# Kernel tuning notes

Measured on AMD Instinct MI355X. Metric: run time of the kernel, lower is better.

Reference implementation:

```python
import jax, jax.numpy as jnp
import numpy as np

B, L, H, N, A = 1024, 50, 256, 100000, 100

def setup_inputs() -> dict:
    key = jax.random.key(0)
    k1, k2, k3, k4, k5, k6 = jax.random.split(key, 6)
    stdv = 1.0 / np.sqrt(H)
    u = lambda k, shp: jax.random.uniform(k, shp, jnp.float32, -stdv, stdv)
    inputs = jax.random.randint(k1, (B, L), 0, N)
    masks = jnp.ones((B, L), jnp.float32)
    return {
        'inputs': inputs,
        'masks': masks,
        'emb': u(k2, (N, H)),
        'Qw': u(k3, (A, H)),
        'Kw': u(k4, (A, H)),
        'lin_w': u(k5, (H, 2 * H)),
        'lin_b': u(k6, (H,)),
    }

def reference(inputs, masks, emb, Qw, Kw, lin_w, lin_b):
    x = emb[inputs]                                   # [B,L,H]
    Q = jax.nn.sigmoid(jnp.einsum('blh,ah->bla', x, Qw))   # [B,L,A]
    K = jax.nn.sigmoid(jnp.einsum('blh,ah->bla', x, Kw))
    affinity = jnp.einsum('bla,bma->blm', Q, K) / jnp.sqrt(jnp.float32(A))  # [B,L,L]
    # remove diagonal (affinity - diag_embed(diagonal))
    eye = jnp.eye(L, dtype=affinity.dtype)
    masked_affinity = affinity * (1.0 - eye)
    col_masked = masked_affinity * masks[:, None, :]  # column mask
    item_score = jnp.sum(col_masked, axis=2) * masks  # [B,L]
    item_score = jax.nn.softmax(item_score, axis=1) * masks
    item_score = item_score / jnp.sum(item_score, axis=1, keepdims=True)
    att_final = jnp.sum(item_score[:, :, None] * x, axis=1)  # [B,H]
    # last valid item per session
    lengths = masks.sum(axis=1).astype(jnp.int32)
    last_id = jnp.take_along_axis(inputs, (lengths - 1)[:, None], axis=1)[:, 0]
    last_emb = emb[last_id]                           # [B,H]
    final_rep = jnp.concatenate([att_final, last_emb], axis=1) @ lin_w.T + lin_b  # [B,H]
    scores = final_rep @ emb[1:].T                    # [B,N-1]
    return scores, affinity
```

## Files before the change

### kernel.cpp

```cpp
#include <hip/hip_runtime.h>
#include <hip/hip_bf16.h>

#define BB 1024
#define LL 50
#define HH 256
#define AA 100
#define NN 100000
#define NM1 99999

typedef short short8 __attribute__((ext_vector_type(8)));
typedef float f32x4 __attribute__((ext_vector_type(4)));

__device__ __forceinline__ float wave_sum(float v) {
#pragma unroll
  for (int off = 32; off; off >>= 1) v += __shfl_xor(v, off, 64);
  return v;
}
__device__ __forceinline__ float wave_max(float v) {
#pragma unroll
  for (int off = 32; off; off >>= 1) v = fmaxf(v, __shfl_xor(v, off, 64));
  return v;
}
__device__ __forceinline__ short f2bf(float f) {
  union { __hip_bfloat16 h; short s; } u;
  u.h = __float2bfloat16(f);
  return u.s;
}
__device__ __forceinline__ float bf2f(short s) {
  union { short s; __hip_bfloat16 h; } u;
  u.s = s;
  return __bfloat162float(u.h);
}

__global__ __launch_bounds__(256) void session_kernel(
    const int* __restrict__ inputs, const float* __restrict__ masks,
    const float* __restrict__ emb, const float* __restrict__ Qw,
    const float* __restrict__ Kw, const float* __restrict__ lin_w,
    const float* __restrict__ lin_b, float* __restrict__ out_aff,
    short* __restrict__ frb) {
  __shared__ short s_xb[64 * 256];
  __shared__ short s_q[64 * 128];
  __shared__ short s_k[64 * 128];
  __shared__ float s_mask[64];
  __shared__ int s_idx[64];
  __shared__ float s_rowp[4][64];
  __shared__ float s_p[64];
  __shared__ float s_cat[2 * HH];
  __shared__ int s_last;

  const int b = blockIdx.x;
  const int tid = threadIdx.x;
  const int lane = tid & 63;
  const int wv = tid >> 6;
  const int l15 = lane & 15;
  const int lg = lane >> 4;

  if (tid < 64) s_mask[tid] = (tid < LL) ? masks[b * LL + tid] : 0.f;
  if (tid < LL) s_idx[tid] = inputs[b * LL + tid];
#pragma unroll
  for (int i = 0; i < 4; ++i) {
    short8 z = {};
    ((short8*)s_q)[tid + i * 256] = z;
    ((short8*)s_k)[tid + i * 256] = z;
  }
  __syncthreads();

  for (int u = tid; u < LL * 32; u += 256) {
    const int r = u >> 5, c = u & 31;
    const float* s = emb + (size_t)s_idx[r] * HH + c * 8;
    const float4 f0 = *(const float4*)s;
    const float4 f1 = *(const float4*)(s + 4);
    short8 v;
    v[0] = f2bf(f0.x); v[1] = f2bf(f0.y); v[2] = f2bf(f0.z); v[3] = f2bf(f0.w);
    v[4] = f2bf(f1.x); v[5] = f2bf(f1.y); v[6] = f2bf(f1.z); v[7] = f2bf(f1.w);
    const int byte = ((r << 9) | (c << 4)) ^ ((r & 7) << 4);
    *(short8*)((char*)s_xb + byte) = v;
  }
  __syncthreads();

  f32x4 acc[4][4];
#pragma unroll
  for (int i = 0; i < 4; ++i)
#pragma unroll
    for (int j = 0; j < 4; ++j) acc[i][j] = (f32x4)(0.f);

#pragma unroll
  for (int ks = 0; ks < 8; ++ks) {
    const int kb = (ks * 32 + lg * 8) * 2;
    short8 af[4];
#pragma unroll
    for (int mf = 0; mf < 4; ++mf) {
      const int r = mf * 16 + l15;
      af[mf] = *(const short8*)((const char*)s_xb +
                                (((r << 9) + kb) ^ ((r & 7) << 4)));
    }
#pragma unroll
    for (int nfi = 0; nfi < 4; ++nfi) {
      const int nf = wv + 4 * nfi;
      const float* Wp = (nf < 7) ? Qw : Kw;
      int arow = (nf < 7) ? nf * 16 + l15 : (nf - 7) * 16 + l15;
      if (nf >= 14) arow = 0;
      if (arow > AA - 1) arow = AA - 1;
      const float* s = Wp + (size_t)arow * HH + ks * 32 + lg * 8;
      const float4 w0 = *(const float4*)s;
      const float4 w1 = *(const float4*)(s + 4);
      short8 bf;
      bf[0] = f2bf(w0.x); bf[1] = f2bf(w0.y); bf[2] = f2bf(w0.z); bf[3] = f2bf(w0.w);
      bf[4] = f2bf(w1.x); bf[5] = f2bf(w1.y); bf[6] = f2bf(w1.z); bf[7] = f2bf(w1.w);
#pragma unroll
      for (int mf = 0; mf < 4; ++mf)
        acc[nfi][mf] =
            __builtin_amdgcn_mfma_f32_16x16x32_bf16(af[mf], bf, acc[nfi][mf], 0, 0, 0);
    }
  }
#pragma unroll
  for (int nfi = 0; nfi < 4; ++nfi) {
    const int nf = wv + 4 * nfi;
#pragma unroll
    for (int mf = 0; mf < 4; ++mf)
#pragma unroll
      for (int j = 0; j < 4; ++j) {
        const int row = mf * 16 + lg * 4 + j;
        const float sg = 1.f / (1.f + expf(-acc[nfi][mf][j]));
        if (row < LL && nf < 14) {
          if (nf < 7) {
            const int a = nf * 16 + l15;
            if (a < AA)
              *(short*)((char*)s_q + (((row << 8) + a * 2) ^ ((row & 7) << 4))) =
                  f2bf(sg);
          } else {
            const int a = (nf - 7) * 16 + l15;
            if (a < AA)
              *(short*)((char*)s_k + (((row << 8) + a * 2) ^ ((row & 7) << 4))) =
                  f2bf(sg);
          }
        }
      }
  }
  __syncthreads();

  f32x4 c4[4];
#pragma unroll
  for (int i = 0; i < 4; ++i) c4[i] = (f32x4)(0.f);
#pragma unroll
  for (int ks = 0; ks < 4; ++ks) {
    const int kb = (ks * 32 + lg * 8) * 2;
    const int mrow = wv * 16 + l15;
    const short8 kf = *(const short8*)((const char*)s_k +
                                       (((mrow << 8) + kb) ^ ((mrow & 7) << 4)));
#pragma unroll
    for (int mf = 0; mf < 4; ++mf) {
      const int r = mf * 16 + l15;
      const short8 qf = *(const short8*)((const char*)s_q +
                                         (((r << 8) + kb) ^ ((r & 7) << 4)));
      c4[mf] = __builtin_amdgcn_mfma_f32_16x16x32_bf16(qf, kf, c4[mf], 0, 0, 0);
    }
  }
  {
    const int col = wv * 16 + l15;
#pragma unroll
    for (int mf = 0; mf < 4; ++mf)
#pragma unroll
      for (int j = 0; j < 4; ++j) {
        const int row = mf * 16 + lg * 4 + j;
        const float val = c4[mf][j] * 0.1f;
        if (row < LL && col < LL)
          out_aff[(size_t)b * (LL * LL) + row * LL + col] = val;
        float am = (col < LL && col != row) ? val * s_mask[col] : 0.f;
        am += __shfl_xor(am, 1, 64);
        am += __shfl_xor(am, 2, 64);
        am += __shfl_xor(am, 4, 64);
        am += __shfl_xor(am, 8, 64);
        if (l15 == 0) s_rowp[wv][row] = am;
      }
  }
  __syncthreads();

  if (tid < 64) {
    const int l = tid;
    const float mk = s_mask[l];
    float v = -3.4e38f;
    if (l < LL)
      v = (s_rowp[0][l] + s_rowp[1][l] + s_rowp[2][l] + s_rowp[3][l]) * mk;
    const float mx = wave_max(v);
    const float e = (l < LL) ? expf(v - mx) : 0.f;
    const float s1 = wave_sum(e);
    float p = e / s1 * mk;
    const float s2 = wave_sum(p);
    p /= s2;
    if (l < LL) s_p[l] = p;
    const float cnt = wave_sum(mk);
    if (l == 0) s_last = s_idx[(int)(cnt + 0.5f) - 1];
  }
  __syncthreads();

  {
    const int h = tid;
    float a = 0.f;
#pragma unroll
    for (int l = 0; l < LL; ++l) {
      const short xv = *(const short*)((const char*)s_xb +
                                       ((((l << 9) + h * 2)) ^ ((l & 7) << 4)));
      a += s_p[l] * bf2f(xv);
    }
    s_cat[h] = a;
    s_cat[HH + h] = emb[(size_t)s_last * HH + h];
  }
  __syncthreads();

  {
    const int h = tid;
    float acc2 = lin_b[h];
    const float4* lw = (const float4*)(lin_w + (size_t)h * (2 * HH));
#pragma unroll 16
    for (int j = 0; j < (2 * HH) / 4; ++j) {
      const float4 w = lw[j];
      const float4 cv = *(const float4*)&s_cat[j * 4];
      acc2 += w.x * cv.x + w.y * cv.y + w.z * cv.z + w.w * cv.w;
    }
    frb[(size_t)b * HH + h] = f2bf(acc2);
  }
}

#define NBLK 782
__global__ __launch_bounds__(256) void scores_kernel(
    const short* __restrict__ frb, const float* __restrict__ emb,
    float* __restrict__ out) {
  __shared__ short As[128 * 128];
  __shared__ short Bs[128 * 128];

  const int tid = threadIdx.x;
  const int wg = blockIdx.x;
  const int p = (wg & 7) * NBLK + (wg >> 3);
  const int m0 = (p & 7) * 128;
  const int n0 = (p >> 3) * 128;

  const int lane = tid & 63;
  const int wv = tid >> 6;
  const int wr = wv >> 1, wc = wv & 1;
  const int l15 = lane & 15, lg = lane >> 4;

  f32x4 acc[4][4];
#pragma unroll
  for (int fm = 0; fm < 4; ++fm)
#pragma unroll
    for (int fn = 0; fn < 4; ++fn) acc[fm][fn] = (f32x4)(0.f);

  for (int kh = 0; kh < 2; ++kh) {
    if (kh) __syncthreads();
#pragma unroll
    for (int i = 0; i < 8; ++i) {
      const int idx = tid + i * 256;
      const int r = idx >> 4, c = idx & 15;
      const int byte = ((r << 8) | (c << 4)) ^ ((r & 7) << 4);
      *(short8*)((char*)As + byte) =
          *(const short8*)(frb + (((size_t)(m0 + r)) << 8) + kh * 128 + (c << 3));
      int er = 1 + n0 + r;
      if (er > NM1) er = NM1;
      const float* s = emb + (((size_t)er) << 8) + kh * 128 + (c << 3);
      const float4 f0 = *(const float4*)s;
      const float4 f1 = *(const float4*)(s + 4);
      short8 v;
      v[0] = f2bf(f0.x); v[1] = f2bf(f0.y); v[2] = f2bf(f0.z); v[3] = f2bf(f0.w);
      v[4] = f2bf(f1.x); v[5] = f2bf(f1.y); v[6] = f2bf(f1.z); v[7] = f2bf(f1.w);
      *(short8*)((char*)Bs + byte) = v;
    }
    __syncthreads();
#pragma unroll
    for (int ks = 0; ks < 4; ++ks) {
      const int kb = ks * 64 + lg * 16;
      short8 af[4], bf[4];
#pragma unroll
      for (int f = 0; f < 4; ++f) {
        const int Ra = wr * 64 + f * 16 + l15;
        af[f] = *(const short8*)((const char*)As +
                                 (((Ra << 8) + kb) ^ ((Ra & 7) << 4)));
        const int Rb = wc * 64 + f * 16 + l15;
        bf[f] = *(const short8*)((const char*)Bs +
                                 (((Rb << 8) + kb) ^ ((Rb & 7) << 4)));
      }
#pragma unroll
      for (int fm = 0; fm < 4; ++fm)
#pragma unroll
        for (int fn = 0; fn < 4; ++fn)
          acc[fm][fn] = __builtin_amdgcn_mfma_f32_16x16x32_bf16(
              af[fm], bf[fn], acc[fm][fn], 0, 0, 0);
    }
  }

#pragma unroll
  for (int fm = 0; fm < 4; ++fm) {
    const int mrow = m0 + wr * 64 + fm * 16 + lg * 4;
#pragma unroll
    for (int fn = 0; fn < 4; ++fn) {
      const int n = n0 + wc * 64 + fn * 16 + l15;
      if (n < NM1) {
#pragma unroll
        for (int j = 0; j < 4; ++j)
          out[(size_t)(mrow + j) * NM1 + n] = acc[fm][fn][j];
      }
    }
  }
}

extern "C" void kernel_launch(void* const* d_in, const int* in_sizes, int n_in,
                              void* d_out, int out_size, void* d_ws,
                              size_t ws_size, hipStream_t stream) {
  const int* inputs = (const int*)d_in[0];
  const float* masks = (const float*)d_in[1];
  const float* emb = (const float*)d_in[2];
  const float* Qw = (const float*)d_in[3];
  const float* Kw = (const float*)d_in[4];
  const float* lin_w = (const float*)d_in[5];
  const float* lin_b = (const float*)d_in[6];

  float* out_scores = (float*)d_out;
  float* out_aff = out_scores + (size_t)BB * NM1;
  short* frb = (short*)d_ws;

  session_kernel<<<dim3(BB), dim3(256), 0, stream>>>(
      inputs, masks, emb, Qw, Kw, lin_w, lin_b, out_aff, frb);

  scores_kernel<<<dim3(8 * NBLK), dim3(256), 0, stream>>>(frb, emb, out_scores);
}
```

Measured before the change: 814.1 us.

## Pre-convert embeddings to bf16 workspace and stream score tiles with register-resident A

The session kernel now also writes a padded bf16 copy of emb[1:] into workspace. A new scores kernel keeps the 128-row final_rep tile in registers and streams several 128-column bf16 embedding tiles straight from global memory into MFMAs, with no LDS staging. The aim is to halve the embedding read traffic and avoid repeated fp32-to-bf16 conversion and LDS round-trips in the large GEMM. The cost is an extra full-table conversion pass and uncoalesced, LDS-free operand loads. It falls back to the old kernel when the workspace is too small.

```diff
diff --git a/kernel.cpp b/kernel.cpp
--- a/kernel.cpp
+++ b/kernel.cpp
@@ -7,6 +7,7 @@
 #define AA 100
 #define NN 100000
 #define NM1 99999
+#define NPAD 100096
 
 typedef short short8 __attribute__((ext_vector_type(8)));
 typedef float f32x4 __attribute__((ext_vector_type(4)));
@@ -37,7 +38,7 @@
     const float* __restrict__ emb, const float* __restrict__ Qw,
     const float* __restrict__ Kw, const float* __restrict__ lin_w,
     const float* __restrict__ lin_b, float* __restrict__ out_aff,
-    short* __restrict__ frb) {
+    short* __restrict__ frb, short* __restrict__ embb) {
   __shared__ short s_xb[64 * 256];
   __shared__ short s_q[64 * 128];
   __shared__ short s_k[64 * 128];
@@ -220,9 +221,95 @@
     }
     frb[(size_t)b * HH + h] = f2bf(acc2);
   }
+
+  if (embb) {
+    const size_t total = (size_t)NPAD * 32;
+    for (size_t u = (size_t)b * 256 + tid; u < total; u += (size_t)BB * 256) {
+      const int r = (int)(u >> 5), c = (int)(u & 31);
+      int er = r + 1;
+      if (er > NM1) er = NM1;
+      const float* s = emb + (size_t)er * HH + c * 8;
+      const float4 f0 = *(const float4*)s;
+      const float4 f1 = *(const float4*)(s + 4);
+      short8 v;
+      v[0] = f2bf(f0.x); v[1] = f2bf(f0.y); v[2] = f2bf(f0.z); v[3] = f2bf(f0.w);
+      v[4] = f2bf(f1.x); v[5] = f2bf(f1.y); v[6] = f2bf(f1.z); v[7] = f2bf(f1.w);
+      *(short8*)(embb + (((size_t)r) << 8) + c * 8) = v;
+    }
+  }
 }
 
 #define NBLK 782
+#define TTILES 4
+#define NCHUNK 196
+__global__ __launch_bounds__(256, 2) void scores_stream(
+    const short* __restrict__ frb, const short* __restrict__ embb,
+    float* __restrict__ out) {
+  const int tid = threadIdx.x;
+  const int bid = blockIdx.x;
+  const int xcd = bid & 7;
+  const int j = bid >> 3;
+  const int cg = (j >> 3) * 8 + xcd;
+  if (cg >= NCHUNK) return;
+  const int m0 = (j & 7) * 128;
+
+  const int lane = tid & 63;
+  const int wv = tid >> 6;
+  const int wr = wv >> 1, wc = wv & 1;
+  const int l15 = lane & 15, lg = lane >> 4;
+
+  short8 af[4][8];
+#pragma unroll
+  for (int fm = 0; fm < 4; ++fm) {
+    const short* ap =
+        frb + (((size_t)(m0 + wr * 64 + fm * 16 + l15)) << 8) + lg * 8;
+#pragma unroll
+    for (int ks = 0; ks < 8; ++ks) af[fm][ks] = *(const short8*)(ap + ks * 32);
+  }
+
+  for (int t = 0; t < TTILES; ++t) {
+    const int nt = cg * TTILES + t;
+    if (nt >= NBLK) break;
+    const int n0 = nt * 128;
+    const short* bp =
+        embb + (((size_t)(n0 + wc * 64 + l15)) << 8) + lg * 8;
+
+    f32x4 acc[4][4];
+#pragma unroll
+    for (int fm = 0; fm < 4; ++fm)
+#pragma unroll
+      for (int fn = 0; fn < 4; ++fn) acc[fm][fn] = (f32x4)(0.f);
+
+#pragma unroll
+    for (int ks = 0; ks < 8; ++ks) {
+      short8 bf[4];
+#pragma unroll
+      for (int fn = 0; fn < 4; ++fn)
+        bf[fn] = *(const short8*)(bp + ((size_t)fn << 12) + ks * 32);
+#pragma unroll
+      for (int fm = 0; fm < 4; ++fm)
+#pragma unroll
+        for (int fn = 0; fn < 4; ++fn)
+          acc[fm][fn] = __builtin_amdgcn_mfma_f32_16x16x32_bf16(
+              af[fm][ks], bf[fn], acc[fm][fn], 0, 0, 0);
+    }
+
+#pragma unroll
+    for (int fm = 0; fm < 4; ++fm) {
+      const int mrow = m0 + wr * 64 + fm * 16 + lg * 4;
+#pragma unroll
+      for (int fn = 0; fn < 4; ++fn) {
+        const int n = n0 + wc * 64 + fn * 16 + l15;
+        if (n < NM1) {
+#pragma unroll
+          for (int jj = 0; jj < 4; ++jj)
+            out[(size_t)(mrow + jj) * NM1 + n] = acc[fm][fn][jj];
+        }
+      }
+    }
+  }
+}
+
 __global__ __launch_bounds__(256) void scores_kernel(
     const short* __restrict__ frb, const float* __restrict__ emb,
     float* __restrict__ out) {
@@ -318,8 +405,17 @@
   float* out_aff = out_scores + (size_t)BB * NM1;
   short* frb = (short*)d_ws;
 
+  const size_t need =
+      (size_t)BB * HH * 2 + (size_t)NPAD * HH * 2;
+  short* embb = (ws_size >= need) ? frb + (size_t)BB * HH : nullptr;
+
   session_kernel<<<dim3(BB), dim3(256), 0, stream>>>(
-      inputs, masks, emb, Qw, Kw, lin_w, lin_b, out_aff, frb);
-
-  scores_kernel<<<dim3(8 * NBLK), dim3(256), 0, stream>>>(frb, emb, out_scores);
-}
+      inputs, masks, emb, Qw, Kw, lin_w, lin_b, out_aff, frb, embb);
+
+  if (embb) {
+    scores_stream<<<dim3(1600), dim3(256), 0, stream>>>(frb, embb, out_scores);
+  } else {
+    scores_kernel<<<dim3(8 * NBLK), dim3(256), 0, stream>>>(frb, emb,
+                                                            out_scores);
+  }
+}
```

Result: no change. 800.4 us (-1.7%).
